# Kernel tuning notes

Measured on AMD Instinct MI355X. Metric: run time of the kernel, lower is better.

## Reference

```python
import math
import jax, jax.numpy as jnp
import numpy as np

R = 6  # number of Hermite functions
EPS = 1e-5  # BatchNorm eps


def setup_inputs() -> dict:
    key = jax.random.key(0)
    k1, k2 = jax.random.split(key)
    B, C, H, W = 8, 64, 128, 128
    out_c = 64
    x = jax.random.normal(k1, (B, C, H, W), dtype=jnp.float32)
    gamma = jnp.ones((C,), dtype=jnp.float32)
    beta = jnp.zeros((C,), dtype=jnp.float32)
    Wt = jax.random.normal(k2, (out_c, C), dtype=jnp.float32) * (1.0 / math.sqrt(C))
    b = jnp.zeros((out_c,), dtype=jnp.float32)
    return {"x": x, "gamma": gamma, "beta": beta, "Wt": Wt, "b": b}


def _hermite_funcs(x):
    # x: (B, C, N) -> psi: (B, C, R, N)
    t = jnp.tanh(x) * math.sqrt(2 * R + 1)
    g = jnp.exp(-t * t / 2)
    pi_q = math.pi ** (-0.25)
    p_prev = pi_q * g                      # psi_0
    p_cur = math.sqrt(2.0) * pi_q * t * g  # psi_1
    ps = [p_prev, p_cur]
    for k in range(2, R):  # tiny fixed loop over recurrence order
        p_next = math.sqrt(2.0 / k) * t * p_cur - math.sqrt((k - 1) / k) * p_prev
        ps.append(p_next)
        p_prev, p_cur = p_cur, p_next
    return jnp.stack(ps, axis=2)


def reference(x, gamma, beta, Wt, b):
    B, C, H, W = x.shape
    xf = x.reshape(B, C, H * W)
    # BatchNorm1d (training-mode batch statistics, biased variance)
    mean = jnp.mean(xf, axis=(0, 2), keepdims=True)
    var = jnp.mean((xf - mean) ** 2, axis=(0, 2), keepdims=True)
    xn = (xf - mean) / jnp.sqrt(var + EPS) * gamma[None, :, None] + beta[None, :, None]
    psi = _hermite_funcs(xn)  # (B, C, R, N)
    cost = jnp.einsum('bikd,bid->bik', psi, xn)
    w = jax.nn.softmax(cost, axis=2)
    y = jnp.einsum('bik,bikd->bid', w, psi)  # (B, C, N)
    out = jnp.einsum('oc,bcd->bod', Wt, y) + b[None, :, None]  # 1x1 conv
    return out.reshape(B, Wt.shape[0], H, W)
```

## Files before the change

kernel.cpp:

```cpp
#include <hip/hip_runtime.h>

typedef short short8 __attribute__((ext_vector_type(8)));
typedef float f32x4 __attribute__((ext_vector_type(4)));

#define NB 8
#define NC 64
#define NN 16384
#define NO 64
#define SQRT13 3.605551275463989f


__device__ __forceinline__ unsigned short f2bf(float f) {
    unsigned int u = __builtin_bit_cast(unsigned int, f);
    u += 0x7fffu + ((u >> 16) & 1u);
    return (unsigned short)(u >> 16);
}

__device__ __forceinline__ unsigned int pack_bf2(float lo, float hi) {
    return (unsigned int)f2bf(lo) | ((unsigned int)f2bf(hi) << 16);
}

__device__ __forceinline__ float tanh13(float x) {
    float e = __expf(2.0f * x);
    float r = __builtin_amdgcn_rcpf(e + 1.0f);
    return fmaf(-2.0f * SQRT13, r, SQRT13);
}

__device__ __forceinline__ float yeval(float xv, float a, float bb,
                                       float c0, float c1, float c2,
                                       float c3, float c4, float c5) {
    float t = tanh13(fmaf(xv, a, bb));
    float gg = __expf(-0.5f * t * t);
    float p = c5;
    p = fmaf(p, t, c4);
    p = fmaf(p, t, c3);
    p = fmaf(p, t, c2);
    p = fmaf(p, t, c1);
    p = fmaf(p, t, c0);
    return gg * p;
}

__global__ __launch_bounds__(256) void k_stats(const float* __restrict__ x,
                                               float* __restrict__ part) {
    int bc = blockIdx.x;
    const float* xp = x + (size_t)bc * NN;
    int tid = threadIdx.x;
    float s = 0.f, ss = 0.f;
    #pragma unroll
    for (int i = 0; i < 16; ++i) {
        float4 v = *(const float4*)(xp + i * 1024 + tid * 4);
        s  += v.x + v.y + v.z + v.w;
        ss += v.x * v.x + v.y * v.y + v.z * v.z + v.w * v.w;
    }
    for (int off = 32; off; off >>= 1) {
        s  += __shfl_down(s, off);
        ss += __shfl_down(ss, off);
    }
    __shared__ float red[2][4];
    int lane = tid & 63, wid = tid >> 6;
    if (lane == 0) { red[0][wid] = s; red[1][wid] = ss; }
    __syncthreads();
    if (tid == 0) {
        part[bc * 2 + 0] = red[0][0] + red[0][1] + red[0][2] + red[0][3];
        part[bc * 2 + 1] = red[1][0] + red[1][1] + red[1][2] + red[1][3];
    }
}

__global__ __launch_bounds__(256) void k_cost(const float* __restrict__ x,
                                              const float* __restrict__ part,
                                              const float* __restrict__ gamma,
                                              const float* __restrict__ beta,
                                              const float* __restrict__ Wt,
                                              float* __restrict__ pp,
                                              unsigned short* __restrict__ WtB) {
    int bc = blockIdx.x;
    int c  = bc & 63;
    int tid = threadIdx.x;

    float s = 0.f, ss = 0.f;
    #pragma unroll
    for (int bb = 0; bb < NB; ++bb) {
        s  += part[(bb * NC + c) * 2 + 0];
        ss += part[(bb * NC + c) * 2 + 1];
    }
    const float inv = 1.0f / (float)(NB * NN);
    float mean = s * inv;
    float var  = ss * inv - mean * mean;
    float istd = 1.0f / sqrtf(var + 1e-5f);
    float a   = gamma[c] * istd;
    float bsh = beta[c] - mean * a;

    const float* xp = x + (size_t)bc * NN;
    float acc[6] = {0.f, 0.f, 0.f, 0.f, 0.f, 0.f};
    #pragma unroll 4
    for (int i = 0; i < 16; ++i) {
        float4 v = *(const float4*)(xp + i * 1024 + tid * 4);
        float xs[4] = {v.x, v.y, v.z, v.w};
        #pragma unroll
        for (int j = 0; j < 4; ++j) {
            float xn = fmaf(xs[j], a, bsh);
            float t = tanh13(xn);
            float g = __expf(-0.5f * t * t);
            float p[6];
            p[0] = 0.7511255444649425f * g;
            p[1] = 1.0622519320271969f * t * g;
            p[2] = t * p[1] - 0.7071067811865476f * p[0];
            p[3] = 0.816496580927726f * (t * p[2] - p[1]);
            p[4] = 0.7071067811865476f * t * p[3] - 0.8660254037844386f * p[2];
            p[5] = 0.6324555320336759f * t * p[4] - 0.8944271909999159f * p[3];
            #pragma unroll
            for (int k = 0; k < 6; ++k) acc[k] = fmaf(p[k], xn, acc[k]);
        }
    }
    __shared__ float red[6][4];
    int lane = tid & 63, wid = tid >> 6;
    #pragma unroll
    for (int k = 0; k < 6; ++k) {
        float v = acc[k];
        for (int off = 32; off; off >>= 1) v += __shfl_down(v, off);
        if (lane == 0) red[k][wid] = v;
    }
    __syncthreads();
    if (tid == 0) {
        float cst[6];
        float mx = -1e30f;
        #pragma unroll
        for (int k = 0; k < 6; ++k) {
            cst[k] = red[k][0] + red[k][1] + red[k][2] + red[k][3];
            mx = fmaxf(mx, cst[k]);
        }
        float sum = 0.f, w[6];
        #pragma unroll
        for (int k = 0; k < 6; ++k) { w[k] = expf(cst[k] - mx); sum += w[k]; }
        float r = 1.0f / sum;
        #pragma unroll
        for (int k = 0; k < 6; ++k) w[k] *= r;

        float h[6][6];
        #pragma unroll
        for (int k = 0; k < 6; ++k)
            #pragma unroll
            for (int j = 0; j < 6; ++j) h[k][j] = 0.f;
        h[0][0] = 0.7511255444649425f;
        h[1][1] = 1.0622519320271969f;
        for (int k = 2; k < 6; ++k) {
            float s2 = sqrtf(2.0f / k), s1 = sqrtf((k - 1.0f) / k);
            for (int j = 5; j >= 0; --j) {
                float v = (j > 0) ? s2 * h[k - 1][j - 1] : 0.f;
                h[k][j] = v - s1 * h[k - 2][j];
            }
        }
        float* P = pp + (size_t)bc * 8;
        P[0] = a; P[1] = bsh;
        #pragma unroll
        for (int j = 0; j < 6; ++j) {
            float v = 0.f;
            #pragma unroll
            for (int k = 0; k < 6; ++k) v += w[k] * h[k][j];
            P[2 + j] = v;
        }
    }
    if (bc == 0) {
        for (int i = tid; i < 4096; i += 256)
            WtB[i] = f2bf(Wt[i]);
    }
}

__global__ __launch_bounds__(256) void k_out(const float* __restrict__ x,
                                             const unsigned short* __restrict__ WtB,
                                             const float* __restrict__ bias,
                                             const float* __restrict__ pp,
                                             float* __restrict__ out) {
    __shared__ float ppl[512];
    int tid  = threadIdx.x;
    int w    = tid >> 6;
    int l    = tid & 63;
    int grp  = l >> 4;
    int ln   = l & 15;
    int b    = blockIdx.x >> 6;
    int tile = blockIdx.x & 63;

    #pragma unroll
    for (int i0 = 0; i0 < 2; ++i0) {
        int i = i0 * 256 + tid;
        ppl[(i & 7) * 64 + (i >> 3)] = pp[(size_t)b * 512 + i];
    }
    __syncthreads();

    short8 af[2][4];
    #pragma unroll
    for (int kk = 0; kk < 2; ++kk)
        #pragma unroll
        for (int mo = 0; mo < 4; ++mo)
            af[kk][mo] = *reinterpret_cast<const short8*>(
                WtB + (mo * 16 + ln) * 64 + kk * 32 + grp * 8);

    f32x4 acc[4][4];
    #pragma unroll
    for (int mo = 0; mo < 4; ++mo)
        #pragma unroll
        for (int nd = 0; nd < 4; ++nd)
            acc[mo][nd] = (f32x4){0.f, 0.f, 0.f, 0.f};

    const float* xb = x + (size_t)b * NC * NN + tile * 256 + w * 64 + ln;

    #pragma unroll
    for (int kk = 0; kk < 2; ++kk) {
        unsigned int bu[4][4];
        #pragma unroll
        for (int q = 0; q < 4; ++q) {
            int c0 = kk * 32 + grp * 8 + 2 * q;
            float A0 = ppl[c0],       A1 = ppl[c0 + 1];
            float B0 = ppl[64 + c0],  B1 = ppl[64 + c0 + 1];
            float p00 = ppl[128 + c0], p01 = ppl[192 + c0], p02 = ppl[256 + c0];
            float p03 = ppl[320 + c0], p04 = ppl[384 + c0], p05 = ppl[448 + c0];
            float p10 = ppl[129 + c0], p11 = ppl[193 + c0], p12 = ppl[257 + c0];
            float p13 = ppl[321 + c0], p14 = ppl[385 + c0], p15 = ppl[449 + c0];
            const float* xc0 = xb + (size_t)c0 * NN;
            const float* xc1 = xc0 + NN;
            #pragma unroll
            for (int nd = 0; nd < 4; ++nd) {
                float y0 = yeval(xc0[nd * 16], A0, B0, p00, p01, p02, p03, p04, p05);
                float y1 = yeval(xc1[nd * 16], A1, B1, p10, p11, p12, p13, p14, p15);
                bu[nd][q] = pack_bf2(y0, y1);
            }
        }
        #pragma unroll
        for (int nd = 0; nd < 4; ++nd) {
            union { unsigned int u[4]; short8 s; } U;
            U.u[0] = bu[nd][0]; U.u[1] = bu[nd][1];
            U.u[2] = bu[nd][2]; U.u[3] = bu[nd][3];
            #pragma unroll
            for (int mo = 0; mo < 4; ++mo)
                acc[mo][nd] = __builtin_amdgcn_mfma_f32_16x16x32_bf16(
                    af[kk][mo], U.s, acc[mo][nd], 0, 0, 0);
        }
    }

    float* ob = out + (size_t)b * NO * NN + tile * 256 + w * 64 + ln;
    #pragma unroll
    for (int mo = 0; mo < 4; ++mo) {
        #pragma unroll
        for (int nd = 0; nd < 4; ++nd) {
            f32x4 v = acc[mo][nd];
            #pragma unroll
            for (int r = 0; r < 4; ++r) {
                int o = mo * 16 + grp * 4 + r;
                ob[(size_t)o * NN + nd * 16] = v[r] + bias[o];
            }
        }
    }
}

extern "C" void kernel_launch(void* const* d_in, const int* in_sizes, int n_in,
                              void* d_out, int out_size, void* d_ws, size_t ws_size,
                              hipStream_t stream) {
    const float* x     = (const float*)d_in[0];
    const float* gamma = (const float*)d_in[1];
    const float* beta  = (const float*)d_in[2];
    const float* Wt    = (const float*)d_in[3];
    const float* bias  = (const float*)d_in[4];
    float* out = (float*)d_out;
    float* ws  = (float*)d_ws;

    float* part = ws;
    float* pp   = ws + 1024;
    unsigned short* WtB = (unsigned short*)(ws + 5120);

    k_stats<<<dim3(NB * NC), dim3(256), 0, stream>>>(x, part);
    k_cost<<<dim3(NB * NC), dim3(256), 0, stream>>>(x, part, gamma, beta, Wt, pp, WtB);
    k_out<<<dim3(NB * NC), dim3(256), 0, stream>>>(x, WtB, bias, pp, out);
}
```

Measured before the change: 37.04 us.

## Accumulate Hermite cost as monomial moments and rebalance stats/cost kernels

The cost reduction now accumulates the moments sum(g*xn*t^k) with a running product and maps them to Hermite costs through the coefficient matrix once per (b,c), which removes the per-element recurrence. k_stats splits each row across two blocks and also does the Wt-to-bf16 conversion. k_cost runs with 512 threads per block. k_out preloads bias as float4 and writes the output with nontemporal stores. The monomial basis adds some floating-point cancellation risk when the moments are combined into costs.

```diff
diff --git a/kernel.cpp b/kernel.cpp
--- a/kernel.cpp
+++ b/kernel.cpp
@@ -41,13 +41,15 @@
 }
 
 __global__ __launch_bounds__(256) void k_stats(const float* __restrict__ x,
-                                               float* __restrict__ part) {
-    int bc = blockIdx.x;
-    const float* xp = x + (size_t)bc * NN;
+                                               float* __restrict__ part,
+                                               const float* __restrict__ Wt,
+                                               unsigned short* __restrict__ WtB) {
+    int blk = blockIdx.x;
+    const float* xp = x + (size_t)(blk >> 1) * NN + (blk & 1) * 8192;
     int tid = threadIdx.x;
     float s = 0.f, ss = 0.f;
     #pragma unroll
-    for (int i = 0; i < 16; ++i) {
+    for (int i = 0; i < 8; ++i) {
         float4 v = *(const float4*)(xp + i * 1024 + tid * 4);
         s  += v.x + v.y + v.z + v.w;
         ss += v.x * v.x + v.y * v.y + v.z * v.z + v.w * v.w;
@@ -61,18 +63,18 @@
     if (lane == 0) { red[0][wid] = s; red[1][wid] = ss; }
     __syncthreads();
     if (tid == 0) {
-        part[bc * 2 + 0] = red[0][0] + red[0][1] + red[0][2] + red[0][3];
-        part[bc * 2 + 1] = red[1][0] + red[1][1] + red[1][2] + red[1][3];
-    }
-}
-
-__global__ __launch_bounds__(256) void k_cost(const float* __restrict__ x,
+        part[blk * 2 + 0] = red[0][0] + red[0][1] + red[0][2] + red[0][3];
+        part[blk * 2 + 1] = red[1][0] + red[1][1] + red[1][2] + red[1][3];
+    }
+    if (blk == 0)
+        for (int i = tid; i < 4096; i += 256) WtB[i] = f2bf(Wt[i]);
+}
+
+__global__ __launch_bounds__(512) void k_cost(const float* __restrict__ x,
                                               const float* __restrict__ part,
                                               const float* __restrict__ gamma,
                                               const float* __restrict__ beta,
-                                              const float* __restrict__ Wt,
-                                              float* __restrict__ pp,
-                                              unsigned short* __restrict__ WtB) {
+                                              float* __restrict__ pp) {
     int bc = blockIdx.x;
     int c  = bc & 63;
     int tid = threadIdx.x;
@@ -80,8 +82,9 @@
     float s = 0.f, ss = 0.f;
     #pragma unroll
     for (int bb = 0; bb < NB; ++bb) {
-        s  += part[(bb * NC + c) * 2 + 0];
-        ss += part[(bb * NC + c) * 2 + 1];
+        int base = ((bb * NC + c) << 1);
+        s  += part[base * 2 + 0] + part[base * 2 + 2];
+        ss += part[base * 2 + 1] + part[base * 2 + 3];
     }
     const float inv = 1.0f / (float)(NB * NN);
     float mean = s * inv;
@@ -91,50 +94,43 @@
     float bsh = beta[c] - mean * a;
 
     const float* xp = x + (size_t)bc * NN;
-    float acc[6] = {0.f, 0.f, 0.f, 0.f, 0.f, 0.f};
+    float m[6] = {0.f, 0.f, 0.f, 0.f, 0.f, 0.f};
     #pragma unroll 4
-    for (int i = 0; i < 16; ++i) {
-        float4 v = *(const float4*)(xp + i * 1024 + tid * 4);
+    for (int i = 0; i < 8; ++i) {
+        float4 v = *(const float4*)(xp + i * 2048 + tid * 4);
         float xs[4] = {v.x, v.y, v.z, v.w};
         #pragma unroll
         for (int j = 0; j < 4; ++j) {
             float xn = fmaf(xs[j], a, bsh);
-            float t = tanh13(xn);
-            float g = __expf(-0.5f * t * t);
-            float p[6];
-            p[0] = 0.7511255444649425f * g;
-            p[1] = 1.0622519320271969f * t * g;
-            p[2] = t * p[1] - 0.7071067811865476f * p[0];
-            p[3] = 0.816496580927726f * (t * p[2] - p[1]);
-            p[4] = 0.7071067811865476f * t * p[3] - 0.8660254037844386f * p[2];
-            p[5] = 0.6324555320336759f * t * p[4] - 0.8944271909999159f * p[3];
-            #pragma unroll
-            for (int k = 0; k < 6; ++k) acc[k] = fmaf(p[k], xn, acc[k]);
-        }
-    }
-    __shared__ float red[6][4];
+            float t  = tanh13(xn);
+            float g  = __expf(-0.5f * t * t);
+            float u  = g * xn;
+            m[0] += u;
+            u *= t; m[1] += u;
+            u *= t; m[2] += u;
+            u *= t; m[3] += u;
+            u *= t; m[4] += u;
+            u *= t; m[5] += u;
+        }
+    }
+    __shared__ float red6[6][8];
     int lane = tid & 63, wid = tid >> 6;
     #pragma unroll
     for (int k = 0; k < 6; ++k) {
-        float v = acc[k];
+        float v = m[k];
         for (int off = 32; off; off >>= 1) v += __shfl_down(v, off);
-        if (lane == 0) red[k][wid] = v;
+        if (lane == 0) red6[k][wid] = v;
     }
     __syncthreads();
     if (tid == 0) {
-        float cst[6];
-        float mx = -1e30f;
+        float M[6];
         #pragma unroll
         for (int k = 0; k < 6; ++k) {
-            cst[k] = red[k][0] + red[k][1] + red[k][2] + red[k][3];
-            mx = fmaxf(mx, cst[k]);
-        }
-        float sum = 0.f, w[6];
-        #pragma unroll
-        for (int k = 0; k < 6; ++k) { w[k] = expf(cst[k] - mx); sum += w[k]; }
-        float r = 1.0f / sum;
-        #pragma unroll
-        for (int k = 0; k < 6; ++k) w[k] *= r;
+            float v = 0.f;
+            #pragma unroll
+            for (int w = 0; w < 8; ++w) v += red6[k][w];
+            M[k] = v;
+        }
 
         float h[6][6];
         #pragma unroll
@@ -150,19 +146,28 @@
                 h[k][j] = v - s1 * h[k - 2][j];
             }
         }
+        float cst[6], mx = -1e30f;
+        #pragma unroll
+        for (int k = 0; k < 6; ++k) {
+            float v = 0.f;
+            #pragma unroll
+            for (int j = 0; j < 6; ++j) v += h[k][j] * M[j];
+            cst[k] = v;
+            mx = fmaxf(mx, v);
+        }
+        float sum = 0.f, w[6];
+        #pragma unroll
+        for (int k = 0; k < 6; ++k) { w[k] = expf(cst[k] - mx); sum += w[k]; }
+        float r = 1.0f / sum;
         float* P = pp + (size_t)bc * 8;
         P[0] = a; P[1] = bsh;
         #pragma unroll
         for (int j = 0; j < 6; ++j) {
             float v = 0.f;
             #pragma unroll
-            for (int k = 0; k < 6; ++k) v += w[k] * h[k][j];
+            for (int k = 0; k < 6; ++k) v += w[k] * r * h[k][j];
             P[2 + j] = v;
         }
-    }
-    if (bc == 0) {
-        for (int i = tid; i < 4096; i += 256)
-            WtB[i] = f2bf(Wt[i]);
     }
 }
 
@@ -195,6 +200,11 @@
             af[kk][mo] = *reinterpret_cast<const short8*>(
                 WtB + (mo * 16 + ln) * 64 + kk * 32 + grp * 8);
 
+    float4 bias4[4];
+    #pragma unroll
+    for (int mo = 0; mo < 4; ++mo)
+        bias4[mo] = *(const float4*)(bias + mo * 16 + grp * 4);
+
     f32x4 acc[4][4];
     #pragma unroll
     for (int mo = 0; mo < 4; ++mo)
@@ -243,11 +253,10 @@
         #pragma unroll
         for (int nd = 0; nd < 4; ++nd) {
             f32x4 v = acc[mo][nd];
-            #pragma unroll
-            for (int r = 0; r < 4; ++r) {
-                int o = mo * 16 + grp * 4 + r;
-                ob[(size_t)o * NN + nd * 16] = v[r] + bias[o];
-            }
+            __builtin_nontemporal_store(v[0] + bias4[mo].x, &ob[(size_t)(mo * 16 + grp * 4 + 0) * NN + nd * 16]);
+            __builtin_nontemporal_store(v[1] + bias4[mo].y, &ob[(size_t)(mo * 16 + grp * 4 + 1) * NN + nd * 16]);
+            __builtin_nontemporal_store(v[2] + bias4[mo].z, &ob[(size_t)(mo * 16 + grp * 4 + 2) * NN + nd * 16]);
+            __builtin_nontemporal_store(v[3] + bias4[mo].w, &ob[(size_t)(mo * 16 + grp * 4 + 3) * NN + nd * 16]);
         }
     }
 }
@@ -264,10 +273,10 @@
     float* ws  = (float*)d_ws;
 
     float* part = ws;
-    float* pp   = ws + 1024;
-    unsigned short* WtB = (unsigned short*)(ws + 5120);
-
-    k_stats<<<dim3(NB * NC), dim3(256), 0, stream>>>(x, part);
-    k_cost<<<dim3(NB * NC), dim3(256), 0, stream>>>(x, part, gamma, beta, Wt, pp, WtB);
+    float* pp   = ws + 2048;
+    unsigned short* WtB = (unsigned short*)(ws + 6144);
+
+    k_stats<<<dim3(2 * NB * NC), dim3(256), 0, stream>>>(x, part, Wt, WtB);
+    k_cost<<<dim3(NB * NC), dim3(512), 0, stream>>>(x, part, gamma, beta, pp);
     k_out<<<dim3(NB * NC), dim3(256), 0, stream>>>(x, WtB, bias, pp, out);
 }
```

Measured after the change: 39.16 us. 1.06x slower.
